# Kernel tuning notes

Measured on AMD Instinct MI355X. Metric: run time of the kernel, lower is better.

Reference implementation:

```python
import jax, jax.numpy as jnp
import numpy as np

N_NODES, N_EDGES, N_ROOTS = 32768, 131072, 1024
VOCAB, EMB_D, FEAT = 50000, 256, 128
SEQ, HEADS, OUT_CH = 16, 16, 125
KERNELS = (5, 6, 7, 8)


def _add_self_loops(edge_index, n):
    loop = jnp.arange(n, dtype=edge_index.dtype)
    src = jnp.concatenate([edge_index[0], loop])
    dst = jnp.concatenate([edge_index[1], loop])
    return src, dst


def _gat_conv(x, W, a_src, a_dst, b, src, dst, n):
    # PyG GATConv (heads=1): h=xW, e_ij = LeakyReLU(a_s.h_j + a_d.h_i), softmax over incoming edges of i
    h = x @ W                                   # [N, F]
    al_s = h @ a_src                            # [N]
    al_d = h @ a_dst                            # [N]
    e = jax.nn.leaky_relu(al_s[src] + al_d[dst], 0.2)   # [E+N]
    m = jax.ops.segment_max(e, dst, num_segments=n)
    ex = jnp.exp(e - m[dst])
    den = jax.ops.segment_sum(ex, dst, num_segments=n)
    coef = ex / den[dst]
    out = jax.ops.segment_sum(coef[:, None] * h[src], dst, num_segments=n)
    return out + b


def _gcn_conv(x, W, b, src, dst, n):
    h = x @ W
    ones = jnp.ones_like(src, dtype=x.dtype)
    deg = jax.ops.segment_sum(ones, dst, num_segments=n)
    dinv = jax.lax.rsqrt(jnp.maximum(deg, 1.0))
    norm = dinv[src] * dinv[dst]                # [E+N]
    out = jax.ops.segment_sum(norm[:, None] * h[src], dst, num_segments=n)
    return out + b


def _transformer_block(x, Wq, bq, Wk, bk, Wv, bv, Wo, bo, g, be):
    # multi-head self-attention + output proj + residual + layernorm (attn_dropout=0)
    n, s, d = x.shape
    dh = d // HEADS
    q = (x @ Wq + bq).reshape(n, s, HEADS, dh)
    k = (x @ Wk + bk).reshape(n, s, HEADS, dh)
    v = (x @ Wv + bv).reshape(n, s, HEADS, dh)
    att = jnp.einsum('nqhd,nkhd->nhqk', q, k) / np.sqrt(dh).astype(np.float32)
    att = jax.nn.softmax(att, axis=-1)
    o = jnp.einsum('nhqk,nkhd->nqhd', att, v).reshape(n, s, d)
    o = o @ Wo + bo
    y = x + o
    mu = jnp.mean(y, axis=-1, keepdims=True)
    var = jnp.var(y, axis=-1, keepdims=True)
    return (y - mu) * jax.lax.rsqrt(var + 1e-5) * g + be


def _conv_branch(t, ws, bs):
    # t: [N, D, S]; Conv1d VALID + ReLU + max-pool over full output length
    feats = []
    for w, b in zip(ws, bs):
        a = jax.lax.conv_general_dilated(t, w, (1,), 'VALID',
                                         dimension_numbers=('NCH', 'OIH', 'NCH'))
        a = jax.nn.relu(a + b[:, None])
        feats.append(jnp.max(a, axis=-1))       # [N, OUT_CH]
    return jnp.concatenate(feats, axis=1)        # [N, 4*OUT_CH]


def _forward(x2, emb, Wq, bq, Wk, bk, Wv, bv, Wo, bo, ln_g, ln_b,
             gat1_W, gat1_as, gat1_ad, gat1_b, gcn1_W, gcn1_b,
             gat2_W, gat2_as, gat2_ad, gat2_b, gcn2_W, gcn2_b,
             conv_w0, conv_b0, conv_w1, conv_b1, conv_w2, conv_b2, conv_w3, conv_b3,
             fc1_W, fc1_b, fc2_W, fc2_b,
             text2, edge_index, root_index, rootpost_index):
    n = x2.shape[0]
    src, dst = _add_self_loops(edge_index, n)

    stance_graph = _gat_conv(x2, gat1_W, gat1_as, gat1_ad, gat1_b, src, dst, n)
    stance_shared = _gcn_conv(x2, gcn1_W, gcn1_b, src, dst, n)

    t = emb[text2]                                            # [N, S, D]
    t = _transformer_block(t, Wq, bq, Wk, bk, Wv, bv, Wo, bo, ln_g, ln_b)
    t_avg = jnp.mean(t, axis=1)                               # [N, D]

    cat = jnp.concatenate([stance_graph, stance_shared, t_avg], axis=1)  # [N, 2F+D]
    stance_graph2 = _gat_conv(cat, gat2_W, gat2_as, gat2_ad, gat2_b, src, dst, n)
    _ = _gcn_conv(stance_shared, gcn2_W, gcn2_b, src, dst, n)  # computed but unused in forward (faithful)

    tc = jnp.transpose(t, (0, 2, 1))                          # [N, D, S]
    text_feat = _conv_branch(tc, (conv_w0, conv_w1, conv_w2, conv_w3),
                             (conv_b0, conv_b1, conv_b2, conv_b3))  # [N, 500]

    final = jnp.concatenate([stance_graph2[root_index],
                             text_feat[root_index],
                             text_feat[rootpost_index]], axis=1)     # [B, F+1000]
    h = jax.nn.relu(final @ fc1_W + fc1_b)
    return h @ fc2_W + fc2_b                                  # [B, 3]


def setup_inputs() -> dict:
    key = jax.random.key(0)
    ks = iter(jax.random.split(key, 48))
    s = 0.05
    inp = {}
    inp['x2'] = jax.random.normal(next(ks), (N_NODES, FEAT), jnp.float32)
    inp['emb'] = jax.random.normal(next(ks), (VOCAB, EMB_D), jnp.float32) * s
    for nm in ['Wq', 'Wk', 'Wv', 'Wo']:
        inp[nm] = jax.random.normal(next(ks), (EMB_D, EMB_D), jnp.float32) * s
    for nm in ['bq', 'bk', 'bv', 'bo']:
        inp[nm] = jnp.zeros((EMB_D,), jnp.float32)
    inp['ln_g'] = jnp.ones((EMB_D,), jnp.float32)
    inp['ln_b'] = jnp.zeros((EMB_D,), jnp.float32)
    inp['gat1_W'] = jax.random.normal(next(ks), (FEAT, FEAT), jnp.float32) * s
    inp['gat1_as'] = jax.random.normal(next(ks), (FEAT,), jnp.float32) * s
    inp['gat1_ad'] = jax.random.normal(next(ks), (FEAT,), jnp.float32) * s
    inp['gat1_b'] = jnp.zeros((FEAT,), jnp.float32)
    inp['gcn1_W'] = jax.random.normal(next(ks), (FEAT, FEAT), jnp.float32) * s
    inp['gcn1_b'] = jnp.zeros((FEAT,), jnp.float32)
    inp['gat2_W'] = jax.random.normal(next(ks), (2 * FEAT + EMB_D, FEAT), jnp.float32) * s
    inp['gat2_as'] = jax.random.normal(next(ks), (FEAT,), jnp.float32) * s
    inp['gat2_ad'] = jax.random.normal(next(ks), (FEAT,), jnp.float32) * s
    inp['gat2_b'] = jnp.zeros((FEAT,), jnp.float32)
    inp['gcn2_W'] = jax.random.normal(next(ks), (FEAT, FEAT), jnp.float32) * s
    inp['gcn2_b'] = jnp.zeros((FEAT,), jnp.float32)
    for i, K in enumerate(KERNELS):
        inp[f'conv_w{i}'] = jax.random.normal(next(ks), (OUT_CH, EMB_D, K), jnp.float32) * s
        inp[f'conv_b{i}'] = jnp.zeros((OUT_CH,), jnp.float32)
    inp['fc1_W'] = jax.random.normal(next(ks), (FEAT + 8 * OUT_CH, 300), jnp.float32) * s
    inp['fc1_b'] = jnp.zeros((300,), jnp.float32)
    inp['fc2_W'] = jax.random.normal(next(ks), (300, 3), jnp.float32) * s
    inp['fc2_b'] = jnp.zeros((3,), jnp.float32)
    inp['text2'] = jax.random.randint(next(ks), (N_NODES, SEQ), 0, VOCAB, jnp.int32)
    inp['edge_index'] = jax.random.randint(next(ks), (2, N_EDGES), 0, N_NODES, jnp.int32)
    inp['root_index'] = jax.random.randint(next(ks), (N_ROOTS,), 0, N_NODES, jnp.int32)
    inp['rootpost_index'] = jax.random.randint(next(ks), (N_ROOTS,), 0, N_NODES, jnp.int32)
    return inp


def reference(x2, emb, Wq, bq, Wk, bk, Wv, bv, Wo, bo, ln_g, ln_b,
              gat1_W, gat1_as, gat1_ad, gat1_b, gcn1_W, gcn1_b,
              gat2_W, gat2_as, gat2_ad, gat2_b, gcn2_W, gcn2_b,
              conv_w0, conv_b0, conv_w1, conv_b1, conv_w2, conv_b2, conv_w3, conv_b3,
              fc1_W, fc1_b, fc2_W, fc2_b,
              text2, edge_index, root_index, rootpost_index):
    return _forward(x2, emb, Wq, bq, Wk, bk, Wv, bv, Wo, bo, ln_g, ln_b,
                    gat1_W, gat1_as, gat1_ad, gat1_b, gcn1_W, gcn1_b,
                    gat2_W, gat2_as, gat2_ad, gat2_b, gcn2_W, gcn2_b,
                    conv_w0, conv_b0, conv_w1, conv_b1, conv_w2, conv_b2, conv_w3, conv_b3,
                    fc1_W, fc1_b, fc2_W, fc2_b,
                    text2, edge_index, root_index, rootpost_index)
```

## Files before the change

### kernel.cpp

```cpp
#include <hip/hip_runtime.h>
#include <hip/hip_bf16.h>
#include <cstdint>
#include <cstddef>

#define N_NODES 32768
#define N_EDGES 131072
#define ET_EDGES (N_EDGES + N_NODES)
#define N_ROOTS 1024
#define EMB_D 256
#define FEAT 128
#define SEQ 16
#define OUT_CH 125

static inline int cdiv(long long a, long long b) { return (int)((a + b - 1) / b); }

typedef short short8 __attribute__((ext_vector_type(8)));
typedef short short4v __attribute__((ext_vector_type(4)));
typedef float f32x4 __attribute__((ext_vector_type(4)));

__device__ __forceinline__ float warpReduceSum(float v) {
#pragma unroll
    for (int m = 32; m; m >>= 1) v += __shfl_xor(v, m, 64);
    return v;
}
__device__ __forceinline__ int encf(float f) {
    int i = __float_as_int(f);
    return i >= 0 ? i : (i ^ 0x7fffffff);
}
__device__ __forceinline__ float decf(int i) {
    return __int_as_float(i >= 0 ? i : (i ^ 0x7fffffff));
}
__device__ __forceinline__ short f2bs(float x) {
    unsigned u = __float_as_uint(x);
    u += 0x7fffu + ((u >> 16) & 1u);
    return (short)(u >> 16);
}
__device__ __forceinline__ short2 f2bs2(float a, float b) {
    union {
        __hip_bfloat162 h;
        short2 s;
    } u;
    u.h = __float22bfloat162_rn(make_float2(a, b));
    return u.s;
}
__device__ __forceinline__ float bs2f(short s) {
    return __uint_as_float(((unsigned)(unsigned short)s) << 16);
}

__global__ void fill_i32(int* p, int v, int n) {
    int i = blockIdx.x * 256 + threadIdx.x;
    if (i < n) p[i] = v;
}

__global__ void init_cat(float* __restrict__ cat, const float* __restrict__ b1, const float* __restrict__ b2) {
    int i = blockIdx.x * 256 + threadIdx.x;
    int n = i >> 8, c = i & 255;
    float b = (c < 128) ? b1[c] : b2[c - 128];
    cat[(size_t)n * 512 + c] = b;
}

__global__ void repack_wall(const float* __restrict__ cw0, const float* __restrict__ cw1,
                            const float* __restrict__ cw2, const float* __restrict__ cw3,
                            __hip_bfloat16* __restrict__ wall) {
    int i = blockIdx.x * 256 + threadIdx.x;
    if (i >= 512 * 2048) return;
    int r = i >> 11, c = i & 2047;
    int k = c >> 8, ic = c & 255;
    float v = 0.f;
    if (r < 500) {
        int Kidx = r / 125, oc = r - Kidx * 125;
        int K = 5 + Kidx;
        if (k < K) {
            const float* cw = Kidx == 0 ? cw0 : Kidx == 1 ? cw1 : Kidx == 2 ? cw2 : cw3;
            v = cw[((size_t)oc * 256 + ic) * K + k];
        }
    }
    wall[i] = __float2bfloat16(v);
}

__global__ void repack_xf(const float* __restrict__ Wq, const float* __restrict__ Wk, const float* __restrict__ Wv,
                          const float* __restrict__ Wo, const float* __restrict__ bq, const float* __restrict__ bk,
                          const float* __restrict__ bv, short* __restrict__ wqkvT, short* __restrict__ woT,
                          float* __restrict__ bqkv) {
    int i = blockIdx.x * 256 + threadIdx.x;
    if (i < 768 * 256) {
        int n = i >> 8, k = i & 255;
        const float* W = n < 256 ? Wq : n < 512 ? Wk : Wv;
        wqkvT[i] = f2bs(W[k * 256 + (n & 255)]);
    }
    if (i < 256 * 256) {
        int n = i >> 8, k = i & 255;
        woT[i] = f2bs(Wo[k * 256 + n]);
    }
    if (i < 768) bqkv[i] = i < 256 ? bq[i] : i < 512 ? bk[i - 256] : bv[i - 512];
}

__global__ void repack_wT(const float* __restrict__ W, short* __restrict__ out, int K, int N) {
    int i = blockIdx.x * 256 + threadIdx.x;
    if (i >= K * N) return;
    int n = i / K, k = i - n * K;
    out[i] = f2bs(W[(size_t)k * N + n]);
}

__global__ __launch_bounds__(256) void mfma_gemm_n128(const float* __restrict__ A, const short* __restrict__ Wt,
                                                      float* __restrict__ C, int K) {
    __shared__ short As[128 * 40];
    __shared__ short Bs[128 * 40];
    const int m0 = blockIdx.x * 128;
    const int tid = threadIdx.x;
    const int lane = tid & 63;
    const int wave = tid >> 6;
    const int wm = (wave >> 1) * 64, wn = (wave & 1) * 64;
    const int quad = lane >> 4, l16 = lane & 15;

    const int r0 = tid >> 2, kc = (tid & 3) * 8;
    const int r1 = r0 + 64;

    f32x4 acc[4][4];
#pragma unroll
    for (int i = 0; i < 4; i++)
#pragma unroll
        for (int j = 0; j < 4; j++) acc[i][j] = (f32x4){0.f, 0.f, 0.f, 0.f};

    for (int k0 = 0; k0 < K; k0 += 32) {
#pragma unroll
        for (int rr = 0; rr < 2; rr++) {
            const int r = rr ? r1 : r0;
            const float* pa = A + (size_t)(m0 + r) * K + k0 + kc;
            float4 a0 = ((const float4*)pa)[0], a1 = ((const float4*)pa)[1];
            short2 c0 = f2bs2(a0.x, a0.y), c1 = f2bs2(a0.z, a0.w), c2 = f2bs2(a1.x, a1.y), c3 = f2bs2(a1.z, a1.w);
            *(short8*)(As + r * 40 + kc) = (short8){c0.x, c0.y, c1.x, c1.y, c2.x, c2.y, c3.x, c3.y};
        }
        *(short8*)(Bs + r0 * 40 + kc) = *(const short8*)(Wt + (size_t)r0 * K + k0 + kc);
        *(short8*)(Bs + r1 * 40 + kc) = *(const short8*)(Wt + (size_t)r1 * K + k0 + kc);
        __syncthreads();
        short8 af[4], bfr[4];
#pragma unroll
        for (int i = 0; i < 4; i++) af[i] = *(const short8*)(As + (wm + i * 16 + l16) * 40 + quad * 8);
#pragma unroll
        for (int j = 0; j < 4; j++) bfr[j] = *(const short8*)(Bs + (wn + j * 16 + l16) * 40 + quad * 8);
#pragma unroll
        for (int i = 0; i < 4; i++)
#pragma unroll
            for (int j = 0; j < 4; j++)
                acc[i][j] = __builtin_amdgcn_mfma_f32_16x16x32_bf16(af[i], bfr[j], acc[i][j], 0, 0, 0);
        __syncthreads();
    }
#pragma unroll
    for (int i = 0; i < 4; i++) {
#pragma unroll
        for (int j = 0; j < 4; j++) {
            const int col = wn + j * 16 + l16;
            const size_t base = (size_t)(m0 + wm + i * 16 + quad * 4) * 128 + col;
#pragma unroll
            for (int r = 0; r < 4; r++) C[base + (size_t)r * 128] = acc[i][j][r];
        }
    }
}

__global__ __launch_bounds__(256) void gemm64(const float* __restrict__ A, const float* __restrict__ B,
                                              const float* __restrict__ bias, float* __restrict__ C,
                                              int M, int N, int K, int lda, int ldc, int doRelu) {
    __shared__ float As[16][65];
    __shared__ float Bs[16][65];
    const int bm = blockIdx.y * 64, bn = blockIdx.x * 64;
    const int tid = threadIdx.x;
    const int tx = tid & 15, ty = tid >> 4;
    float acc[4][4] = {};
    for (int k0 = 0; k0 < K; k0 += 16) {
#pragma unroll
        for (int j = 0; j < 4; j++) {
            int i = tid + j * 256;
            int kk = i & 15, m = i >> 4;
            int gr = bm + m, gc = k0 + kk;
            As[kk][m] = (gr < M && gc < K) ? A[(size_t)gr * lda + gc] : 0.f;
        }
#pragma unroll
        for (int j = 0; j < 4; j++) {
            int i = tid + j * 256;
            int n = i & 63, kk = i >> 6;
            int gr = k0 + kk, gc = bn + n;
            Bs[kk][n] = (gr < K && gc < N) ? B[(size_t)gr * N + gc] : 0.f;
        }
        __syncthreads();
#pragma unroll
        for (int kk = 0; kk < 16; kk++) {
            float a[4], b[4];
#pragma unroll
            for (int i2 = 0; i2 < 4; i2++) a[i2] = As[kk][ty * 4 + i2];
#pragma unroll
            for (int j2 = 0; j2 < 4; j2++) b[j2] = Bs[kk][tx * 4 + j2];
#pragma unroll
            for (int i2 = 0; i2 < 4; i2++)
#pragma unroll
                for (int j2 = 0; j2 < 4; j2++) acc[i2][j2] = fmaf(a[i2], b[j2], acc[i2][j2]);
        }
        __syncthreads();
    }
#pragma unroll
    for (int i2 = 0; i2 < 4; i2++) {
        int r = bm + ty * 4 + i2;
        if (r >= M) continue;
#pragma unroll
        for (int j2 = 0; j2 < 4; j2++) {
            int c = bn + tx * 4 + j2;
            if (c >= N) continue;
            float v = acc[i2][j2];
            if (bias) v += bias[c];
            if (doRelu) v = fmaxf(v, 0.f);
            C[(size_t)r * ldc + c] = v;
        }
    }
}

__global__ __launch_bounds__(256) void alpha_kernel(const float* __restrict__ h, const float* __restrict__ asrc,
                                                    const float* __restrict__ adst, float* __restrict__ als,
                                                    float* __restrict__ ald) {
    int gw = (blockIdx.x * 256 + threadIdx.x) >> 6;
    int lane = threadIdx.x & 63;
    if (gw >= N_NODES) return;
    const float* row = h + (size_t)gw * FEAT;
    float v0 = row[lane], v1 = row[lane + 64];
    float ps = v0 * asrc[lane] + v1 * asrc[lane + 64];
    float pd = v0 * adst[lane] + v1 * adst[lane + 64];
    ps = warpReduceSum(ps);
    pd = warpReduceSum(pd);
    if (lane == 0) {
        als[gw] = ps;
        ald[gw] = pd;
    }
}

__device__ __forceinline__ void edge_decode(int i, const int* __restrict__ ei, int& s, int& d) {
    if (i < N_EDGES) {
        s = ei[i];
        d = ei[N_EDGES + i];
    } else {
        s = d = i - N_EDGES;
    }
}

__global__ void edge_p1(const int* __restrict__ ei, const float* __restrict__ als, const float* __restrict__ ald,
                        float* __restrict__ elog, int* __restrict__ menc, float* dega) {
    int i = blockIdx.x * 256 + threadIdx.x;
    if (i >= ET_EDGES) return;
    int s, d;
    edge_decode(i, ei, s, d);
    float e = als[s] + ald[d];
    e = (e >= 0.f) ? e : 0.2f * e;
    elog[i] = e;
    atomicMax(&menc[d], encf(e));
    if (dega) unsafeAtomicAdd(&dega[d], 1.f);
}

__global__ void edge_p2(const int* __restrict__ ei, float* __restrict__ elog, const int* __restrict__ menc,
                        float* __restrict__ den) {
    int i = blockIdx.x * 256 + threadIdx.x;
    if (i >= ET_EDGES) return;
    int s, d;
    edge_decode(i, ei, s, d);
    float ex = __expf(elog[i] - decf(menc[d]));
    elog[i] = ex;
    unsafeAtomicAdd(&den[d], ex);
}

__global__ void edge_p2b(const int* __restrict__ ei, float* __restrict__ elog, const float* __restrict__ den) {
    int i = blockIdx.x * 256 + threadIdx.x;
    if (i >= ET_EDGES) return;
    int s, d;
    edge_decode(i, ei, s, d);
    elog[i] = elog[i] / den[d];
}

__global__ void dinv_kernel(float* deg) {
    int i = blockIdx.x * 256 + threadIdx.x;
    if (i < N_NODES) deg[i] = rsqrtf(fmaxf(deg[i], 1.f));
}

__global__ void edge_scatter(const int* __restrict__ ei, const float* __restrict__ coef, const float* __restrict__ h,
                             float* __restrict__ out, int ldo) {
    int i = blockIdx.x * 256 + threadIdx.x;
    if (i >= ET_EDGES * FEAT) return;
    int e = i >> 7, f = i & 127;
    int s, d;
    edge_decode(e, ei, s, d);
    unsafeAtomicAdd(&out[(size_t)d * ldo + f], coef[e] * h[(size_t)s * FEAT + f]);
}

__global__ void gcn_scatter(const int* __restrict__ ei, const float* __restrict__ dinv, const float* __restrict__ h,
                            float* __restrict__ out, int ldo) {
    int i = blockIdx.x * 256 + threadIdx.x;
    if (i >= ET_EDGES * FEAT) return;
    int e = i >> 7, f = i & 127;
    int s, d;
    edge_decode(e, ei, s, d);
    float coef = dinv[s] * dinv[d];
    unsafeAtomicAdd(&out[(size_t)d * ldo + f], coef * h[(size_t)s * FEAT + f]);
}

__global__ void root_gather(const float* __restrict__ g2, const int* __restrict__ rooti, const float* __restrict__ gb,
                            float* __restrict__ fin) {
    int i = blockIdx.x * 256 + threadIdx.x;
    if (i >= N_ROOTS * FEAT) return;
    int r = i >> 7, c = i & 127;
    fin[(size_t)r * 1128 + c] = g2[(size_t)rooti[r] * FEAT + c] + gb[c];
}

__global__ void fc2_kernel(const float* __restrict__ fch, const float* __restrict__ W, const float* __restrict__ b,
                           float* __restrict__ out) {
    int i = blockIdx.x * 256 + threadIdx.x;
    if (i >= N_ROOTS * 3) return;
    int r = i / 3, c = i - r * 3;
    float acc = b[c];
    for (int k = 0; k < 300; k++) acc = fmaf(fch[(size_t)r * 300 + k], W[k * 3 + c], acc);
    out[i] = acc;
}

#define QA_STRIDE 264
#define KR_STRIDE 264

__device__ __forceinline__ int vt_addr(int d, int key) {
    return d * 32 + (((key & 24) ^ (((d ^ (d >> 2)) & 3) << 3)) | (key & 7));
}

template <int MODE>
__global__ __launch_bounds__(256, 4) void xformer_kernel(
    const float* __restrict__ emb, const int* __restrict__ text2, const short* __restrict__ wqkvT,
    const float* __restrict__ bqkv, const short* __restrict__ woT, const float* __restrict__ bo,
    const float* __restrict__ lng, const float* __restrict__ lnb, const int* __restrict__ rooti,
    const int* __restrict__ rpi, float* __restrict__ cat, unsigned short* __restrict__ tbuf) {
    __shared__ short qa[32 * QA_STRIDE];
    __shared__ short kreg[32 * KR_STRIDE];

    const int tid = threadIdx.x;
    const int wave = tid >> 6, lane = tid & 63;
    const int quad = lane >> 4, l16 = lane & 15;

    int gnode[2];
#pragma unroll
    for (int m = 0; m < 2; m++) {
        int slot = blockIdx.x * 2 + m;
        gnode[m] = (MODE == 0) ? slot : ((slot < N_ROOTS) ? rooti[slot] : rpi[slot - N_ROOTS]);
    }

    {
        const int row = tid >> 3, seg = tid & 7;
        const int m = row >> 4, r = row & 15;
        const int tok = text2[gnode[m] * SEQ + r];
        const float* ep = emb + (size_t)tok * 256 + seg * 32;
#pragma unroll
        for (int j = 0; j < 4; j++) {
            float4 ea = ((const float4*)(ep + j * 8))[0];
            float4 eb = ((const float4*)(ep + j * 8))[1];
            short2 w0 = f2bs2(ea.x, ea.y), w1 = f2bs2(ea.z, ea.w);
            short2 w2 = f2bs2(eb.x, eb.y), w3 = f2bs2(eb.z, eb.w);
            *(short8*)(kreg + row * KR_STRIDE + seg * 32 + j * 8) =
                (short8){w0.x, w0.y, w1.x, w1.y, w2.x, w2.y, w3.x, w3.y};
        }
    }
    __syncthreads();

    auto run_gemm = [&](const short* __restrict__ W, int wrow0, const short* __restrict__ Albase,
                        f32x4(&acc)[4][2]) {
#pragma unroll
        for (int i = 0; i < 4; i++) {
            acc[i][0] = (f32x4){0.f, 0.f, 0.f, 0.f};
            acc[i][1] = (f32x4){0.f, 0.f, 0.f, 0.f};
        }
        const short* wb = W + (size_t)(wrow0 + l16) * 256 + quad * 8;
        short8 Bcur[4], Bnxt[4];
#pragma unroll
        for (int i = 0; i < 4; i++) Bcur[i] = *(const short8*)(wb + (size_t)i * 16 * 256);
#pragma unroll
        for (int k0 = 0; k0 < 8; k0++) {
            if (k0 < 7) {
#pragma unroll
                for (int i = 0; i < 4; i++)
                    Bnxt[i] = *(const short8*)(wb + (size_t)i * 16 * 256 + (k0 + 1) * 32);
            }
            short8 A0 = *(const short8*)(Albase + l16 * KR_STRIDE + k0 * 32 + quad * 8);
            short8 A1 = *(const short8*)(Albase + (16 + l16) * KR_STRIDE + k0 * 32 + quad * 8);
#pragma unroll
            for (int i = 0; i < 4; i++) {
                acc[i][0] = __builtin_amdgcn_mfma_f32_16x16x32_bf16(A0, Bcur[i], acc[i][0], 0, 0, 0);
                acc[i][1] = __builtin_amdgcn_mfma_f32_16x16x32_bf16(A1, Bcur[i], acc[i][1], 0, 0, 0);
            }
#pragma unroll
            for (int i = 0; i < 4; i++) Bcur[i] = Bnxt[i];
        }
    };

    f32x4 vacc[4][2];
    {
        f32x4 acc[4][2];
        run_gemm(wqkvT, (0 * 16 + wave * 4) * 16, kreg, acc);
#pragma unroll
        for (int i = 0; i < 4; i++) {
            const int col = (wave * 4 + i) * 16 + l16;
            const float b = bqkv[col];
#pragma unroll
            for (int m = 0; m < 2; m++) {
                const int rbase = m * 16 + quad * 4;
                short2 p01 = f2bs2((acc[i][m][0] + b) * 0.25f, (acc[i][m][1] + b) * 0.25f);
                short2 p23 = f2bs2((acc[i][m][2] + b) * 0.25f, (acc[i][m][3] + b) * 0.25f);
                qa[(rbase + 0) * QA_STRIDE + col] = p01.x;
                qa[(rbase + 1) * QA_STRIDE + col] = p01.y;
                qa[(rbase + 2) * QA_STRIDE + col] = p23.x;
                qa[(rbase + 3) * QA_STRIDE + col] = p23.y;
            }
        }
        run_gemm(wqkvT, (2 * 16 + wave * 4) * 16, kreg, vacc);
#pragma unroll
        for (int i = 0; i < 4; i++) {
            const float b = bqkv[(2 * 16 + wave * 4 + i) * 16 + l16];
#pragma unroll
            for (int m = 0; m < 2; m++)
#pragma unroll
                for (int r = 0; r < 4; r++) vacc[i][m][r] += b;
        }
        f32x4 kacc[4][2];
        run_gemm(wqkvT, (1 * 16 + wave * 4) * 16, kreg, kacc);
        __syncthreads();
#pragma unroll
        for (int i = 0; i < 4; i++) {
            const int colg = (1 * 16 + wave * 4 + i) * 16 + l16;
            const float b = bqkv[colg];
            const int cl = colg - 256;
#pragma unroll
            for (int m = 0; m < 2; m++) {
                const int rbase = m * 16 + quad * 4;
                short2 p01 = f2bs2(kacc[i][m][0] + b, kacc[i][m][1] + b);
                short2 p23 = f2bs2(kacc[i][m][2] + b, kacc[i][m][3] + b);
                kreg[(rbase + 0) * KR_STRIDE + cl] = p01.x;
                kreg[(rbase + 1) * KR_STRIDE + cl] = p01.y;
                kreg[(rbase + 2) * KR_STRIDE + cl] = p23.x;
                kreg[(rbase + 3) * KR_STRIDE + cl] = p23.y;
            }
        }
    }

#pragma unroll
    for (int p = 0; p < 2; p++) {
#pragma unroll
        for (int i = 0; i < 4; i++) {
            const int h = wave * 4 + i;
            const int arow = p * 16 + l16;
            const int q8 = (quad & 1) * 8;
            short8 Af = *(const short8*)(kreg + arow * KR_STRIDE + h * 16 + q8);
            short8 Bf = *(const short8*)(qa + arow * QA_STRIDE + h * 16 + q8);
            if (quad >= 2) {
                Af = (short8){0, 0, 0, 0, 0, 0, 0, 0};
                Bf = (short8){0, 0, 0, 0, 0, 0, 0, 0};
            }
            f32x4 S = __builtin_amdgcn_mfma_f32_16x16x32_bf16(Af, Bf, (f32x4){0.f, 0.f, 0.f, 0.f}, 0, 0, 0);
            float mx = fmaxf(fmaxf(S[0], S[1]), fmaxf(S[2], S[3]));
            mx = fmaxf(mx, __shfl_xor(mx, 16));
            mx = fmaxf(mx, __shfl_xor(mx, 32));
            float e0 = __expf(S[0] - mx), e1 = __expf(S[1] - mx);
            float e2 = __expf(S[2] - mx), e3 = __expf(S[3] - mx);
            float sm = (e0 + e1) + (e2 + e3);
            sm += __shfl_xor(sm, 16);
            sm += __shfl_xor(sm, 32);
            const float inv = 1.f / sm;
            short2 p01 = f2bs2(e0 * inv, e1 * inv), p23 = f2bs2(e2 * inv, e3 * inv);
            *(short4v*)(qa + arow * QA_STRIDE + h * 16 + quad * 4) = (short4v){p01.x, p01.y, p23.x, p23.y};
        }
    }
    __syncthreads();

#pragma unroll
    for (int i = 0; i < 4; i++) {
        const int d = (wave * 4 + i) * 16 + l16;
#pragma unroll
        for (int m = 0; m < 2; m++) {
            const int rbase = m * 16 + quad * 4;
            short2 p01 = f2bs2(vacc[i][m][0], vacc[i][m][1]), p23 = f2bs2(vacc[i][m][2], vacc[i][m][3]);
            *(short4v*)(kreg + vt_addr(d, rbase)) = (short4v){p01.x, p01.y, p23.x, p23.y};
        }
    }

#pragma unroll
    for (int p = 0; p < 2; p++) {
#pragma unroll
        for (int i = 0; i < 4; i++) {
            const int h = wave * 4 + i;
            const int arow = p * 16 + l16;
            const int q8 = (quad & 1) * 8;
            short8 BP = *(const short8*)(qa + arow * QA_STRIDE + h * 16 + q8);
            short8 Av = *(const short8*)(kreg + vt_addr(h * 16 + l16, p * 16 + q8));
            if (quad >= 2) {
                BP = (short8){0, 0, 0, 0, 0, 0, 0, 0};
                Av = (short8){0, 0, 0, 0, 0, 0, 0, 0};
            }
            f32x4 O = __builtin_amdgcn_mfma_f32_16x16x32_bf16(Av, BP, (f32x4){0.f, 0.f, 0.f, 0.f}, 0, 0, 0);
            short2 o01 = f2bs2(O[0], O[1]), o23 = f2bs2(O[2], O[3]);
            *(short4v*)(qa + arow * QA_STRIDE + h * 16 + quad * 4) = (short4v){o01.x, o01.y, o23.x, o23.y};
        }
    }
    __syncthreads();

    {
        f32x4 oacc[4][2];
        run_gemm(woT, (wave * 4) * 16, qa, oacc);
#pragma unroll
        for (int i = 0; i < 4; i++) {
            const int col = (wave * 4 + i) * 16 + l16;
            const float bocol = bo[col];
#pragma unroll
            for (int m = 0; m < 2; m++) {
                const int rbase = m * 16 + quad * 4;
                short2 a01 = f2bs2(oacc[i][m][0] + bocol, oacc[i][m][1] + bocol);
                short2 a23 = f2bs2(oacc[i][m][2] + bocol, oacc[i][m][3] + bocol);
                kreg[(rbase + 0) * KR_STRIDE + col] = a01.x;
                kreg[(rbase + 1) * KR_STRIDE + col] = a01.y;
                kreg[(rbase + 2) * KR_STRIDE + col] = a23.x;
                kreg[(rbase + 3) * KR_STRIDE + col] = a23.y;
            }
        }
    }
    __syncthreads();

    float* qs = (float*)qa;
    {
        const int row = tid >> 3, seg = tid & 7;
        const int m = row >> 4, r = row & 15;
        const int tokr = text2[gnode[m] * SEQ + r];
        const float* ep = emb + (size_t)tokr * 256 + seg * 32;
        float sum = 0.f, sq = 0.f;
#pragma unroll
        for (int j = 0; j < 4; j++) {
            short8 y8 = *(const short8*)(kreg + row * KR_STRIDE + seg * 32 + j * 8);
            float4 ea = ((const float4*)(ep + j * 8))[0];
            float4 eb = ((const float4*)(ep + j * 8))[1];
            float ev[8] = {ea.x, ea.y, ea.z, ea.w, eb.x, eb.y, eb.z, eb.w};
            float yv[8];
#pragma unroll
            for (int e = 0; e < 8; e++) {
                yv[e] = bs2f(y8[e]) + ev[e];
                sum += yv[e];
                sq = fmaf(yv[e], yv[e], sq);
            }
            short2 w0 = f2bs2(yv[0], yv[1]), w1 = f2bs2(yv[2], yv[3]);
            short2 w2 = f2bs2(yv[4], yv[5]), w3 = f2bs2(yv[6], yv[7]);
            *(short4v*)(kreg + row * KR_STRIDE + seg * 32 + j * 8) = (short4v){w0.x, w0.y, w1.x, w1.y};
            *(short4v*)(kreg + row * KR_STRIDE + seg * 32 + j * 8 + 4) = (short4v){w2.x, w2.y, w3.x, w3.y};
        }
        qs[tid] = sum;
        qs[256 + tid] = sq;
    }
    __syncthreads();
    if (tid < 32) {
        float s = 0.f, q2 = 0.f;
#pragma unroll
        for (int j = 0; j < 8; j++) {
            s += qs[tid * 8 + j];
            q2 += qs[256 + tid * 8 + j];
        }
        float mu = s * (1.f / 256.f);
        float var = q2 * (1.f / 256.f) - mu * mu;
        qs[512 + tid * 2] = mu;
        qs[512 + tid * 2 + 1] = rsqrtf(var + 1e-5f);
    }
    __syncthreads();
    {
        const int c = tid;
        const float g = lng[c], bb = lnb[c];
        float csum[2] = {0.f, 0.f};
#pragma unroll
        for (int m = 0; m < 2; m++) {
#pragma unroll
            for (int r = 0; r < 16; r++) {
                const int row = m * 16 + r;
                const float yv = bs2f(kreg[row * KR_STRIDE + c]);
                const float mu = qs[512 + row * 2], rstd = qs[512 + row * 2 + 1];
                const float o = (yv - mu) * rstd * g + bb;
                if (MODE == 0) {
                    csum[m] += o;
                } else {
                    tbuf[((size_t)(blockIdx.x * 2 + m) * 24 + r) * 256 + c] = (unsigned short)f2bs(o);
                }
            }
        }
        if (MODE == 0) {
            cat[(size_t)gnode[0] * 512 + 256 + c] = csum[0] * (1.f / 16.f);
            cat[(size_t)gnode[1] * 512 + 256 + c] = csum[1] * (1.f / 16.f);
        } else {
            for (int z = tid; z < 2 * 8 * 256; z += 256) {
                const int m = z >> 11, rem = z & 2047;
                tbuf[((size_t)(blockIdx.x * 2 + m) * 24 + 16 + (rem >> 8)) * 256 + (rem & 255)] = 0;
            }
        }
    }
}

__global__ __launch_bounds__(256) void conv_gemm(const short* __restrict__ tb, const short* __restrict__ wall,
                                                 float* __restrict__ C) {
    __shared__ short As[128 * 40];
    __shared__ short Bs[128 * 40];
    const int bid = blockIdx.x;
    const int m0 = (bid >> 2) * 128;
    const int n0 = (bid & 3) * 128;
    const int tid = threadIdx.x;
    const int lane = tid & 63;
    const int wave = tid >> 6;
    const int wm = (wave >> 1) * 64, wn = (wave & 1) * 64;
    const int quad = lane >> 4, l16 = lane & 15;

    const int r0 = tid >> 2, kc = (tid & 3) * 8;
    const int r1 = r0 + 64;
    const int am0 = m0 + r0, am1 = m0 + r1;
    const int s0 = am0 / 12, p0_ = am0 - s0 * 12;
    const int s1 = am1 / 12, p1_ = am1 - s1 * 12;
    const size_t ga0 = (size_t)(s0 * 24 + p0_) * 256 + kc;
    const size_t ga1 = (size_t)(s1 * 24 + p1_) * 256 + kc;
    const size_t gb0 = (size_t)(n0 + r0) * 2048 + kc;
    const size_t gb1 = (size_t)(n0 + r1) * 2048 + kc;
    short* sa0 = As + r0 * 40 + kc;
    short* sa1 = As + r1 * 40 + kc;
    short* sb0 = Bs + r0 * 40 + kc;
    short* sb1 = Bs + r1 * 40 + kc;

    f32x4 acc[4][4];
#pragma unroll
    for (int i = 0; i < 4; i++)
#pragma unroll
        for (int j = 0; j < 4; j++) acc[i][j] = (f32x4){0.f, 0.f, 0.f, 0.f};

    for (int k0 = 0; k0 < 2048; k0 += 32) {
        short8 a0 = *(const short8*)(tb + ga0 + k0);
        short8 a1 = *(const short8*)(tb + ga1 + k0);
        short8 b0 = *(const short8*)(wall + gb0 + k0);
        short8 b1 = *(const short8*)(wall + gb1 + k0);
        *(short8*)sa0 = a0;
        *(short8*)sa1 = a1;
        *(short8*)sb0 = b0;
        *(short8*)sb1 = b1;
        __syncthreads();
        short8 af[4], bfr[4];
#pragma unroll
        for (int i = 0; i < 4; i++) af[i] = *(const short8*)(As + (wm + i * 16 + l16) * 40 + quad * 8);
#pragma unroll
        for (int j = 0; j < 4; j++) bfr[j] = *(const short8*)(Bs + (wn + j * 16 + l16) * 40 + quad * 8);
#pragma unroll
        for (int i = 0; i < 4; i++)
#pragma unroll
            for (int j = 0; j < 4; j++)
                acc[i][j] = __builtin_amdgcn_mfma_f32_16x16x32_bf16(af[i], bfr[j], acc[i][j], 0, 0, 0);
        __syncthreads();
    }
#pragma unroll
    for (int i = 0; i < 4; i++) {
#pragma unroll
        for (int j = 0; j < 4; j++) {
            const int col = n0 + wn + j * 16 + l16;
            const size_t base = (size_t)(m0 + wm + i * 16 + quad * 4) * 512 + col;
#pragma unroll
            for (int r = 0; r < 4; r++) C[base + (size_t)r * 512] = acc[i][j][r];
        }
    }
}

__global__ void conv_maxpool(const float* __restrict__ C, const float* __restrict__ cb0, const float* __restrict__ cb1,
                             const float* __restrict__ cb2, const float* __restrict__ cb3, float* __restrict__ fin) {
    int i = blockIdx.x * 256 + threadIdx.x;
    if (i >= 2048 * 500) return;
    int slot = i / 500, q = i - slot * 500;
    int Kidx = q / 125, oc = q - Kidx * 125;
    int L = 12 - Kidx;
    const float* base = C + (size_t)(slot * 12) * 512 + q;
    float m = base[0];
    for (int p = 1; p < L; p++) m = fmaxf(m, base[(size_t)p * 512]);
    float b = (Kidx == 0 ? cb0 : Kidx == 1 ? cb1 : Kidx == 2 ? cb2 : cb3)[oc];
    float v = fmaxf(m + b, 0.f);
    int idx = slot < N_ROOTS ? slot : slot - N_ROOTS;
    int colbase = slot < N_ROOTS ? 128 : 628;
    fin[(size_t)idx * 1128 + colbase + q] = v;
}

extern "C" void kernel_launch(void* const* d_in, const int* in_sizes, int n_in, void* d_out, int out_size, void* d_ws,
                              size_t ws_size, hipStream_t stream) {
    const float* x2 = (const float*)d_in[0];
    const float* emb = (const float*)d_in[1];
    const float* Wq = (const float*)d_in[2];
    const float* Wk = (const float*)d_in[3];
    const float* Wv = (const float*)d_in[4];
    const float* Wo = (const float*)d_in[5];
    const float* bq = (const float*)d_in[6];
    const float* bk = (const float*)d_in[7];
    const float* bv = (const float*)d_in[8];
    const float* bo = (const float*)d_in[9];
    const float* lng = (const float*)d_in[10];
    const float* lnb = (const float*)d_in[11];
    const float* gat1_W = (const float*)d_in[12];
    const float* gat1_as = (const float*)d_in[13];
    const float* gat1_ad = (const float*)d_in[14];
    const float* gat1_b = (const float*)d_in[15];
    const float* gcn1_W = (const float*)d_in[16];
    const float* gcn1_b = (const float*)d_in[17];
    const float* gat2_W = (const float*)d_in[18];
    const float* gat2_as = (const float*)d_in[19];
    const float* gat2_ad = (const float*)d_in[20];
    const float* gat2_b = (const float*)d_in[21];
    const float* cw0 = (const float*)d_in[24];
    const float* cb0 = (const float*)d_in[25];
    const float* cw1 = (const float*)d_in[26];
    const float* cb1 = (const float*)d_in[27];
    const float* cw2 = (const float*)d_in[28];
    const float* cb2 = (const float*)d_in[29];
    const float* cw3 = (const float*)d_in[30];
    const float* cb3 = (const float*)d_in[31];
    const float* fc1_W = (const float*)d_in[32];
    const float* fc1_b = (const float*)d_in[33];
    const float* fc2_W = (const float*)d_in[34];
    const float* fc2_b = (const float*)d_in[35];
    const int* text2 = (const int*)d_in[36];
    const int* ei = (const int*)d_in[37];
    const int* rooti = (const int*)d_in[38];
    const int* rpi = (const int*)d_in[39];

    float* ws = (float*)d_ws;
    size_t off = 0;
    auto alloc = [&](size_t n) {
        float* p = ws + off;
        off += n;
        return p;
    };
    float* g2o = alloc((size_t)N_NODES * FEAT);
    float* den1 = alloc(N_NODES);
    float* den2 = alloc(N_NODES);
    float* deg = alloc(N_NODES);
    size_t zero_floats = off;
    float* cat = alloc((size_t)N_NODES * 512);
    float* h1 = alloc((size_t)N_NODES * FEAT);
    float* h2 = alloc((size_t)N_NODES * FEAT);
    float* hg2 = alloc((size_t)N_NODES * FEAT);
    float* als1 = alloc(N_NODES);
    float* ald1 = alloc(N_NODES);
    float* als2 = alloc(N_NODES);
    float* ald2 = alloc(N_NODES);
    int* m1 = (int*)alloc(N_NODES);
    int* m2 = (int*)alloc(N_NODES);
    float* el1 = alloc(ET_EDGES);
    float* el2 = alloc(ET_EDGES);
    float* fin = alloc((size_t)N_ROOTS * 1128);
    float* fch = alloc((size_t)N_ROOTS * 300);
    float* wallf = alloc(512 * 2048 / 2);
    float* wqkvTf = alloc(768 * 256 / 2);
    float* woTf = alloc(256 * 256 / 2);
    float* bqkv = alloc(768);
    float* wg1Tf = alloc(128 * 128 / 2);
    float* wc1Tf = alloc(128 * 128 / 2);
    float* wg2Tf = alloc(128 * 512 / 2);
    (void)ws_size;
    (void)in_sizes;
    (void)n_in;
    (void)out_size;

    unsigned short* tbuf = (unsigned short*)h1;
    __hip_bfloat16* wall = (__hip_bfloat16*)wallf;
    short* wqkvT = (short*)wqkvTf;
    short* woT = (short*)woTf;
    short* wg1T = (short*)wg1Tf;
    short* wc1T = (short*)wc1Tf;
    short* wg2T = (short*)wg2Tf;
    float* Cbuf = cat;

    hipMemsetAsync(g2o, 0, zero_floats * sizeof(float), stream);
    init_cat<<<cdiv((long long)N_NODES * 256, 256), 256, 0, stream>>>(cat, gat1_b, gcn1_b);
    fill_i32<<<cdiv(2 * N_NODES, 256), 256, 0, stream>>>(m1, (int)0x80000000, 2 * N_NODES);
    repack_wall<<<cdiv(512 * 2048, 256), 256, 0, stream>>>(cw0, cw1, cw2, cw3, wall);
    repack_xf<<<cdiv(768 * 256, 256), 256, 0, stream>>>(Wq, Wk, Wv, Wo, bq, bk, bv, wqkvT, woT, bqkv);
    repack_wT<<<cdiv(128 * 128, 256), 256, 0, stream>>>(gat1_W, wg1T, 128, 128);
    repack_wT<<<cdiv(128 * 128, 256), 256, 0, stream>>>(gcn1_W, wc1T, 128, 128);
    repack_wT<<<cdiv(512 * 128, 256), 256, 0, stream>>>(gat2_W, wg2T, 512, 128);

    mfma_gemm_n128<<<N_NODES / 128, 256, 0, stream>>>(x2, wg1T, h1, 128);
    mfma_gemm_n128<<<N_NODES / 128, 256, 0, stream>>>(x2, wc1T, h2, 128);
    alpha_kernel<<<cdiv((long long)N_NODES * 64, 256), 256, 0, stream>>>(h1, gat1_as, gat1_ad, als1, ald1);
    edge_p1<<<cdiv(ET_EDGES, 256), 256, 0, stream>>>(ei, als1, ald1, el1, m1, deg);
    edge_p2<<<cdiv(ET_EDGES, 256), 256, 0, stream>>>(ei, el1, m1, den1);
    edge_p2b<<<cdiv(ET_EDGES, 256), 256, 0, stream>>>(ei, el1, den1);
    dinv_kernel<<<cdiv(N_NODES, 256), 256, 0, stream>>>(deg);
    const int sc_blocks = cdiv((long long)ET_EDGES * FEAT, 256);
    edge_scatter<<<sc_blocks, 256, 0, stream>>>(ei, el1, h1, cat + 0, 512);
    gcn_scatter<<<sc_blocks, 256, 0, stream>>>(ei, deg, h2, cat + 128, 512);
    xformer_kernel<0><<<N_NODES / 2, 256, 0, stream>>>(emb, text2, wqkvT, bqkv, woT, bo, lng, lnb, rooti, rpi, cat,
                                                       nullptr);
    xformer_kernel<1><<<2 * N_ROOTS / 2, 256, 0, stream>>>(emb, text2, wqkvT, bqkv, woT, bo, lng, lnb, rooti, rpi,
                                                           nullptr, tbuf);
    mfma_gemm_n128<<<N_NODES / 128, 256, 0, stream>>>(cat, wg2T, hg2, 512);
    alpha_kernel<<<cdiv((long long)N_NODES * 64, 256), 256, 0, stream>>>(hg2, gat2_as, gat2_ad, als2, ald2);
    edge_p1<<<cdiv(ET_EDGES, 256), 256, 0, stream>>>(ei, als2, ald2, el2, m2, nullptr);
    edge_p2<<<cdiv(ET_EDGES, 256), 256, 0, stream>>>(ei, el2, m2, den2);
    edge_p2b<<<cdiv(ET_EDGES, 256), 256, 0, stream>>>(ei, el2, den2);
    edge_scatter<<<sc_blocks, 256, 0, stream>>>(ei, el2, hg2, g2o, FEAT);
    conv_gemm<<<192 * 4, 256, 0, stream>>>((const short*)tbuf, (const short*)wall, Cbuf);
    root_gather<<<cdiv(N_ROOTS * FEAT, 256), 256, 0, stream>>>(g2o, rooti, gat2_b, fin);
    conv_maxpool<<<cdiv(2048 * 500, 256), 256, 0, stream>>>(Cbuf, cb0, cb1, cb2, cb3, fin);
    gemm64<<<dim3(cdiv(300, 64), cdiv(N_ROOTS, 64)), 256, 0, stream>>>(fin, fc1_W, fc1_b, fch, N_ROOTS, 300, 1128,
                                                                       1128, 300, 1);
    fc2_kernel<<<cdiv(N_ROOTS * 3, 256), 256, 0, stream>>>(fch, fc2_W, fc2_b, (float*)d_out);
}
```

Measured before the change: 2.105 ms.

## Swizzle transformer LDS tiles, keep embeddings in registers, raise occupancy

```diff
diff --git a/kernel.cpp b/kernel.cpp
--- a/kernel.cpp
+++ b/kernel.cpp
@@ -316,21 +316,22 @@
     out[i] = acc;
 }
 
-#define QA_STRIDE 264
-#define KR_STRIDE 264
+__device__ __forceinline__ int lsw(int row, int col) {
+    return row * 256 + (col ^ ((row & 7) << 3));
+}
 
 __device__ __forceinline__ int vt_addr(int d, int key) {
     return d * 32 + (((key & 24) ^ (((d ^ (d >> 2)) & 3) << 3)) | (key & 7));
 }
 
 template <int MODE>
-__global__ __launch_bounds__(256, 4) void xformer_kernel(
+__global__ __launch_bounds__(256, 5) void xformer_kernel(
     const float* __restrict__ emb, const int* __restrict__ text2, const short* __restrict__ wqkvT,
     const float* __restrict__ bqkv, const short* __restrict__ woT, const float* __restrict__ bo,
     const float* __restrict__ lng, const float* __restrict__ lnb, const int* __restrict__ rooti,
     const int* __restrict__ rpi, float* __restrict__ cat, unsigned short* __restrict__ tbuf) {
-    __shared__ short qa[32 * QA_STRIDE];
-    __shared__ short kreg[32 * KR_STRIDE];
+    __shared__ short qa[32 * 256];
+    __shared__ short kreg[32 * 256];
 
     const int tid = threadIdx.x;
     const int wave = tid >> 6, lane = tid & 63;
@@ -342,6 +343,8 @@
         int slot = blockIdx.x * 2 + m;
         gnode[m] = (MODE == 0) ? slot : ((slot < N_ROOTS) ? rooti[slot] : rpi[slot - N_ROOTS]);
     }
+
+    float4 ev[8];
 
     {
         const int row = tid >> 3, seg = tid & 7;
@@ -352,9 +355,11 @@
         for (int j = 0; j < 4; j++) {
             float4 ea = ((const float4*)(ep + j * 8))[0];
             float4 eb = ((const float4*)(ep + j * 8))[1];
+            ev[j * 2] = ea;
+            ev[j * 2 + 1] = eb;
             short2 w0 = f2bs2(ea.x, ea.y), w1 = f2bs2(ea.z, ea.w);
             short2 w2 = f2bs2(eb.x, eb.y), w3 = f2bs2(eb.z, eb.w);
-            *(short8*)(kreg + row * KR_STRIDE + seg * 32 + j * 8) =
+            *(short8*)(kreg + lsw(row, seg * 32 + j * 8)) =
                 (short8){w0.x, w0.y, w1.x, w1.y, w2.x, w2.y, w3.x, w3.y};
         }
     }
@@ -378,8 +383,8 @@
                 for (int i = 0; i < 4; i++)
                     Bnxt[i] = *(const short8*)(wb + (size_t)i * 16 * 256 + (k0 + 1) * 32);
             }
-            short8 A0 = *(const short8*)(Albase + l16 * KR_STRIDE + k0 * 32 + quad * 8);
-            short8 A1 = *(const short8*)(Albase + (16 + l16) * KR_STRIDE + k0 * 32 + quad * 8);
+            short8 A0 = *(const short8*)(Albase + lsw(l16, k0 * 32 + quad * 8));
+            short8 A1 = *(const short8*)(Albase + lsw(16 + l16, k0 * 32 + quad * 8));
 #pragma unroll
             for (int i = 0; i < 4; i++) {
                 acc[i][0] = __builtin_amdgcn_mfma_f32_16x16x32_bf16(A0, Bcur[i], acc[i][0], 0, 0, 0);
@@ -403,10 +408,10 @@
                 const int rbase = m * 16 + quad * 4;
                 short2 p01 = f2bs2((acc[i][m][0] + b) * 0.25f, (acc[i][m][1] + b) * 0.25f);
                 short2 p23 = f2bs2((acc[i][m][2] + b) * 0.25f, (acc[i][m][3] + b) * 0.25f);
-                qa[(rbase + 0) * QA_STRIDE + col] = p01.x;
-                qa[(rbase + 1) * QA_STRIDE + col] = p01.y;
-                qa[(rbase + 2) * QA_STRIDE + col] = p23.x;
-                qa[(rbase + 3) * QA_STRIDE + col] = p23.y;
+                qa[lsw(rbase + 0, col)] = p01.x;
+                qa[lsw(rbase + 1, col)] = p01.y;
+                qa[lsw(rbase + 2, col)] = p23.x;
+                qa[lsw(rbase + 3, col)] = p23.y;
             }
         }
         run_gemm(wqkvT, (2 * 16 + wave * 4) * 16, kreg, vacc);
@@ -431,10 +436,10 @@
                 const int rbase = m * 16 + quad * 4;
                 short2 p01 = f2bs2(kacc[i][m][0] + b, kacc[i][m][1] + b);
                 short2 p23 = f2bs2(kacc[i][m][2] + b, kacc[i][m][3] + b);
-                kreg[(rbase + 0) * KR_STRIDE + cl] = p01.x;
-                kreg[(rbase + 1) * KR_STRIDE + cl] = p01.y;
-                kreg[(rbase + 2) * KR_STRIDE + cl] = p23.x;
-                kreg[(rbase + 3) * KR_STRIDE + cl] = p23.y;
+                kreg[lsw(rbase + 0, cl)] = p01.x;
+                kreg[lsw(rbase + 1, cl)] = p01.y;
+                kreg[lsw(rbase + 2, cl)] = p23.x;
+                kreg[lsw(rbase + 3, cl)] = p23.y;
             }
         }
     }
@@ -446,8 +451,8 @@
             const int h = wave * 4 + i;
             const int arow = p * 16 + l16;
             const int q8 = (quad & 1) * 8;
-            short8 Af = *(const short8*)(kreg + arow * KR_STRIDE + h * 16 + q8);
-            short8 Bf = *(const short8*)(qa + arow * QA_STRIDE + h * 16 + q8);
+            short8 Af = *(const short8*)(kreg + lsw(arow, h * 16 + q8));
+            short8 Bf = *(const short8*)(qa + lsw(arow, h * 16 + q8));
             if (quad >= 2) {
                 Af = (short8){0, 0, 0, 0, 0, 0, 0, 0};
                 Bf = (short8){0, 0, 0, 0, 0, 0, 0, 0};
@@ -463,7 +468,7 @@
             sm += __shfl_xor(sm, 32);
             const float inv = 1.f / sm;
             short2 p01 = f2bs2(e0 * inv, e1 * inv), p23 = f2bs2(e2 * inv, e3 * inv);
-            *(short4v*)(qa + arow * QA_STRIDE + h * 16 + quad * 4) = (short4v){p01.x, p01.y, p23.x, p23.y};
+            *(short4v*)(qa + lsw(arow, h * 16 + quad * 4)) = (short4v){p01.x, p01.y, p23.x, p23.y};
         }
     }
     __syncthreads();
@@ -486,7 +491,7 @@
             const int h = wave * 4 + i;
             const int arow = p * 16 + l16;
             const int q8 = (quad & 1) * 8;
-            short8 BP = *(const short8*)(qa + arow * QA_STRIDE + h * 16 + q8);
+            short8 BP = *(const short8*)(qa + lsw(arow, h * 16 + q8));
             short8 Av = *(const short8*)(kreg + vt_addr(h * 16 + l16, p * 16 + q8));
             if (quad >= 2) {
                 BP = (short8){0, 0, 0, 0, 0, 0, 0, 0};
@@ -494,7 +499,7 @@
             }
             f32x4 O = __builtin_amdgcn_mfma_f32_16x16x32_bf16(Av, BP, (f32x4){0.f, 0.f, 0.f, 0.f}, 0, 0, 0);
             short2 o01 = f2bs2(O[0], O[1]), o23 = f2bs2(O[2], O[3]);
-            *(short4v*)(qa + arow * QA_STRIDE + h * 16 + quad * 4) = (short4v){o01.x, o01.y, o23.x, o23.y};
+            *(short4v*)(qa + lsw(arow, h * 16 + quad * 4)) = (short4v){o01.x, o01.y, o23.x, o23.y};
         }
     }
     __syncthreads();
@@ -511,10 +516,10 @@
                 const int rbase = m * 16 + quad * 4;
                 short2 a01 = f2bs2(oacc[i][m][0] + bocol, oacc[i][m][1] + bocol);
                 short2 a23 = f2bs2(oacc[i][m][2] + bocol, oacc[i][m][3] + bocol);
-                kreg[(rbase + 0) * KR_STRIDE + col] = a01.x;
-                kreg[(rbase + 1) * KR_STRIDE + col] = a01.y;
-                kreg[(rbase + 2) * KR_STRIDE + col] = a23.x;
-                kreg[(rbase + 3) * KR_STRIDE + col] = a23.y;
+                kreg[lsw(rbase + 0, col)] = a01.x;
+                kreg[lsw(rbase + 1, col)] = a01.y;
+                kreg[lsw(rbase + 2, col)] = a23.x;
+                kreg[lsw(rbase + 3, col)] = a23.y;
             }
         }
     }
@@ -523,27 +528,25 @@
     float* qs = (float*)qa;
     {
         const int row = tid >> 3, seg = tid & 7;
-        const int m = row >> 4, r = row & 15;
-        const int tokr = text2[gnode[m] * SEQ + r];
-        const float* ep = emb + (size_t)tokr * 256 + seg * 32;
         float sum = 0.f, sq = 0.f;
 #pragma unroll
         for (int j = 0; j < 4; j++) {
-            short8 y8 = *(const short8*)(kreg + row * KR_STRIDE + seg * 32 + j * 8);
-            float4 ea = ((const float4*)(ep + j * 8))[0];
-            float4 eb = ((const float4*)(ep + j * 8))[1];
-            float ev[8] = {ea.x, ea.y, ea.z, ea.w, eb.x, eb.y, eb.z, eb.w};
+            const int base = lsw(row, seg * 32 + j * 8);
+            short8 y8 = *(const short8*)(kreg + base);
+            float4 ea = ev[j * 2];
+            float4 eb = ev[j * 2 + 1];
+            float evv[8] = {ea.x, ea.y, ea.z, ea.w, eb.x, eb.y, eb.z, eb.w};
             float yv[8];
 #pragma unroll
             for (int e = 0; e < 8; e++) {
-                yv[e] = bs2f(y8[e]) + ev[e];
+                yv[e] = bs2f(y8[e]) + evv[e];
                 sum += yv[e];
                 sq = fmaf(yv[e], yv[e], sq);
             }
             short2 w0 = f2bs2(yv[0], yv[1]), w1 = f2bs2(yv[2], yv[3]);
             short2 w2 = f2bs2(yv[4], yv[5]), w3 = f2bs2(yv[6], yv[7]);
-            *(short4v*)(kreg + row * KR_STRIDE + seg * 32 + j * 8) = (short4v){w0.x, w0.y, w1.x, w1.y};
-            *(short4v*)(kreg + row * KR_STRIDE + seg * 32 + j * 8 + 4) = (short4v){w2.x, w2.y, w3.x, w3.y};
+            *(short4v*)(kreg + base) = (short4v){w0.x, w0.y, w1.x, w1.y};
+            *(short4v*)(kreg + base + 4) = (short4v){w2.x, w2.y, w3.x, w3.y};
         }
         qs[tid] = sum;
         qs[256 + tid] = sq;
@@ -571,7 +574,7 @@
 #pragma unroll
             for (int r = 0; r < 16; r++) {
                 const int row = m * 16 + r;
-                const float yv = bs2f(kreg[row * KR_STRIDE + c]);
+                const float yv = bs2f(kreg[lsw(row, c)]);
                 const float mu = qs[512 + row * 2], rstd = qs[512 + row * 2 + 1];
                 const float o = (yv - mu) * rstd * g + bb;
                 if (MODE == 0) {
```

After: 2.479 ms. 17.8% more time.
